# Performance work log

Hardware: AMD Instinct MI355X
Metric: run time of the kernel (lower is better)

Reference implementation:

```python
import jax, jax.numpy as jnp
import numpy as np

NQ = 4  # n_qubits_per_head


def _apply_ry(state, theta, q):
    # state: (N, 2,2,2,2) real amplitudes; theta: (N,) per-element angle; wire q
    st = jnp.moveaxis(state, 1 + q, -1)
    c = jnp.cos(0.5 * theta).reshape(-1, 1, 1, 1)
    s = jnp.sin(0.5 * theta).reshape(-1, 1, 1, 1)
    a0, a1 = st[..., 0], st[..., 1]
    st = jnp.stack([c * a0 - s * a1, s * a0 + c * a1], axis=-1)
    return jnp.moveaxis(st, -1, 1 + q)


def _apply_cnot(state, ctrl, tgt):
    st = jnp.moveaxis(state, (1 + ctrl, 1 + tgt), (-2, -1))
    st = jnp.stack([st[..., 0, :], st[..., 1, ::-1]], axis=-2)
    return jnp.moveaxis(st, (-2, -1), (1 + ctrl, 1 + tgt))


def _quantum_circuit(x_in, par):
    # x_in: (N, NQ) data angles; par: (N, L, NQ) variational angles (per head, tiled)
    N = x_in.shape[0]
    L = par.shape[1]
    state = jnp.zeros((N, 2, 2, 2, 2), x_in.dtype).at[:, 0, 0, 0, 0].set(1.0)
    for l in range(L):
        for q in range(NQ):
            state = _apply_ry(state, par[:, l, q], q)
        for q in range(NQ - 1):
            state = _apply_cnot(state, q, q + 1)
        state = _apply_cnot(state, NQ - 1, 0)
    for q in range(NQ):
        state = _apply_ry(state, x_in[:, q], q)
    p = state * state  # probabilities (real amplitudes: only RY/CNOT gates)
    zs = []
    for q in range(NQ):
        st = jnp.moveaxis(p, 1 + q, -1)
        zs.append(jnp.sum(st[..., 0], axis=(1, 2, 3)) - jnp.sum(st[..., 1], axis=(1, 2, 3)))
    return jnp.stack(zs, axis=-1)  # (N, NQ)


def setup_inputs() -> dict:
    key = jax.random.key(0)
    ks = jax.random.split(key, 6)
    B, T, E, H, L = 4, 2048, 1024, 16, 2
    scale = 1.0 / np.sqrt(E)
    x = jax.random.normal(ks[0], (B, T, E), dtype=jnp.float32)
    Wq = jax.random.normal(ks[1], (E, E), dtype=jnp.float32) * scale
    Wk = jax.random.normal(ks[2], (E, E), dtype=jnp.float32) * scale
    Wv = jax.random.normal(ks[3], (E, E), dtype=jnp.float32) * scale
    Wo = jax.random.normal(ks[4], (E, E), dtype=jnp.float32) * scale
    qparams = jax.random.normal(ks[5], (H, L, NQ), dtype=jnp.float32)
    return {"x": x, "Wq": Wq, "Wk": Wk, "Wv": Wv, "Wo": Wo, "qparams": qparams}


def reference(x, Wq, Wk, Wv, Wo, qparams):
    B, T, E = x.shape
    H, L, _ = qparams.shape
    hd = E // H
    q = x @ Wq.T
    k = x @ Wk.T
    v = x @ Wv.T
    # NOTE: original scales by sqrt(embed_dim), not sqrt(head_dim)
    scores = jnp.einsum('bte,bse->bts', q, k) / jnp.sqrt(jnp.asarray(E, x.dtype))
    w = jax.nn.softmax(scores, axis=-1)
    out = jnp.einsum('bts,bse->bte', w, v)
    oh = out.reshape(B, T, H, hd)
    N = B * T * H
    xin = oh[..., :NQ].reshape(N, NQ)
    par = jnp.broadcast_to(qparams[None, None], (B, T, H, L, NQ)).reshape(N, L, NQ)
    z = _quantum_circuit(xin, par)  # (N, NQ)
    zfull = jnp.concatenate([z, jnp.zeros((N, hd - NQ), x.dtype)], axis=-1)
    return zfull.reshape(B, T, E) @ Wo.T
```

## Files before the change

kernel.cpp:

```cpp
#include <hip/hip_runtime.h>
#include <hip/hip_fp16.h>

typedef _Float16 half_t;
typedef __attribute__((ext_vector_type(4))) _Float16 half4;
typedef __attribute__((ext_vector_type(8))) _Float16 half8;
typedef __attribute__((ext_vector_type(4))) float floatx4;

__device__ __forceinline__ void async_copy16(const void* src, void* dst_lds) {
  __builtin_amdgcn_global_load_lds(
      (__attribute__((address_space(1))) void*)src,
      (__attribute__((address_space(3))) void*)dst_lds, 16, 0, 0);
}

__global__ __launch_bounds__(512, 2) void gemm_nt_256(
    const half_t* __restrict__ A, const half_t* __restrict__ B,
    half_t* __restrict__ C,
    int lda, int ldb, int ldc, int kIters,
    long sAz2, long sBz2, long sCz2, float scale)
{
  __shared__ __align__(16) half_t sm[2][2][256 * 64];

  const int tid  = threadIdx.x;
  const int wave = tid >> 6, lane = tid & 63;
  const int wm = wave >> 2, wn = wave & 3;
  const int er = lane >> 4, ec = lane & 15;
  const int sw = ec & 7;

  const long z = blockIdx.z;
  const half_t* Ab = A + (long)blockIdx.x * 256 * lda + z * sAz2;
  const half_t* Bb = B + (long)blockIdx.y * 256 * ldb + z * sBz2;

  const int srow = tid >> 3;
  const int skq  = (tid & 7) ^ (srow & 7);

  floatx4 acc[2][2][4][2];
  #pragma unroll
  for (int a = 0; a < 2; a++)
    #pragma unroll
    for (int b = 0; b < 2; b++)
      #pragma unroll
      for (int i = 0; i < 4; i++)
        #pragma unroll
        for (int j = 0; j < 2; j++)
          acc[a][b][i][j] = (floatx4){0.f, 0.f, 0.f, 0.f};

#define STAGE_A(bb, hf, kt) do {                                              \
    const half_t* Ak_ = Ab + (long)(kt) * 64;                                 \
    _Pragma("unroll")                                                         \
    for (int r_ = 0; r_ < 2; r_++) {                                          \
      int lrow_ = r_ * 64 + srow;                                             \
      async_copy16(Ak_ + (long)((hf) * 128 + lrow_) * lda + skq * 8,          \
                   &sm[(bb)][0][(hf) * 8192 + (r_ * 512 + wave * 64) * 8]);   \
    } } while (0)

#define STAGE_B(bb, hf, kt) do {                                              \
    const half_t* Bk_ = Bb + (long)(kt) * 64;                                 \
    _Pragma("unroll")                                                         \
    for (int r_ = 0; r_ < 2; r_++) {                                          \
      int lrow_ = r_ * 64 + srow;                                             \
      async_copy16(Bk_ + (long)((hf) * 128 + lrow_) * ldb + skq * 8,          \
                   &sm[(bb)][1][(hf) * 8192 + (r_ * 512 + wave * 64) * 8]);   \
    } } while (0)

#define DS_A(DST, BB, MH, KS) do {                                            \
    _Pragma("unroll")                                                         \
    for (int ii = 0; ii < 4; ii++) {                                          \
      int row_ = (MH) * 128 + wm * 64 + ii * 16 + ec;                         \
      DST[ii] = *(const half8*)                                               \
          &sm[BB][0][row_ * 64 + ((((KS) * 4 + er) ^ sw) * 8)];               \
    } } while (0)

#define DS_B(DST, BB, KS) do {                                                \
    _Pragma("unroll")                                                         \
    for (int nj = 0; nj < 4; nj++) {                                          \
      int row_ = (nj >> 1) * 128 + wn * 32 + (nj & 1) * 16 + ec;              \
      DST[nj] = *(const half8*)                                               \
          &sm[BB][1][row_ * 64 + ((((KS) * 4 + er) ^ sw) * 8)];               \
    } } while (0)

#define MFMA16(AF, BF, MH) do {                                               \
    __builtin_amdgcn_s_setprio(1);                                            \
    _Pragma("unroll")                                                         \
    for (int ii = 0; ii < 4; ii++)                                            \
      _Pragma("unroll")                                                       \
      for (int nj = 0; nj < 4; nj++)                                          \
        acc[MH][nj >> 1][ii][nj & 1] =                                        \
            __builtin_amdgcn_mfma_f32_16x16x32_f16(                           \
                AF[ii], BF[nj], acc[MH][nj >> 1][ii][nj & 1], 0, 0, 0);       \
    __builtin_amdgcn_s_setprio(0);                                            \
  } while (0)

#define BAR() __builtin_amdgcn_s_barrier()
#define VMW(N) asm volatile("s_waitcnt vmcnt(" #N ")" ::: "memory")

  half8 afA[4], afB[4], bfA[4], bfB[4];
  int cur = 0;
  const int nt = kIters;

  STAGE_B(0, 0, 0); STAGE_B(0, 1, 0); STAGE_A(0, 0, 0); STAGE_A(0, 1, 0);
  VMW(2);
  BAR();
  DS_A(afA, 0, 0, 0);
  DS_B(bfA, 0, 0);

  for (int n = 0; n < nt; ++n) {
    const int hasNext = (n + 1 < nt);
    DS_A(afB, cur, 0, 1);
    DS_B(bfB, cur, 1);
    if (hasNext) { STAGE_B(cur ^ 1, 0, n + 1); STAGE_B(cur ^ 1, 1, n + 1); }
    MFMA16(afA, bfA, 0);
    if (hasNext) { VMW(4); } else { VMW(0); }
    BAR();
    DS_A(afA, cur, 1, 0);
    if (hasNext) STAGE_A(cur ^ 1, 0, n + 1);
    MFMA16(afB, bfB, 0);
    BAR();
    DS_A(afB, cur, 1, 1);
    if (hasNext) STAGE_A(cur ^ 1, 1, n + 1);
    MFMA16(afA, bfA, 1);
    if (hasNext) VMW(2);
    BAR();
    if (hasNext) {
      DS_A(afA, cur ^ 1, 0, 0);
      DS_B(bfA, cur ^ 1, 0);
    }
    MFMA16(afB, bfB, 1);
    BAR();
    cur ^= 1;
  }

#undef STAGE_A
#undef STAGE_B
#undef DS_A
#undef DS_B
#undef MFMA16
#undef BAR
#undef VMW

  const long rowBase = (long)blockIdx.x * 256;
  const long colBase = (long)blockIdx.y * 256;
  half_t* Cz = C + z * sCz2;
  #pragma unroll
  for (int mh = 0; mh < 2; mh++)
    #pragma unroll
    for (int nh = 0; nh < 2; nh++)
      #pragma unroll
      for (int ii = 0; ii < 4; ii++)
        #pragma unroll
        for (int jj = 0; jj < 2; jj++)
          #pragma unroll
          for (int r = 0; r < 4; r++) {
            long row = rowBase + mh * 128 + wm * 64 + ii * 16 + er * 4 + r;
            long col = colBase + nh * 128 + wn * 32 + jj * 16 + ec;
            Cz[row * (long)ldc + col] =
                (_Float16)(acc[mh][nh][ii][jj][r] * scale);
          }
}

template<int BN, int EPI>
__global__ __launch_bounds__(256) void gemm_nt(
    const half_t* __restrict__ A, const half_t* __restrict__ B,
    void* __restrict__ Cout,
    int lda, int ldb, int ldc, int kIters, int zShift,
    long sAz1, long sBz1, long sCz1,
    long sAz2, long sBz2, long sCz2, float scale,
    const float* __restrict__ qab)
{
  constexpr int BM = 128;
  constexpr int WN = BN / 2;
  constexpr int AN = WN / 16;
  constexpr int RA = BM * 8 / 256;
  constexpr int RB = BN * 8 / 256;
  __shared__ __align__(16) half_t lA[BM * 64];
  __shared__ __align__(16) half_t lB[BN * 64];

  const int tid  = threadIdx.x;
  const int wave = tid >> 6, lane = tid & 63;
  const int wm = wave >> 1, wn = wave & 1;
  const int er = lane >> 4, ec = lane & 15;
  const int sw = ec & 7;

  const long z = blockIdx.z;
  const long z2 = z >> zShift;
  const long z1 = z - (z2 << zShift);
  const half_t* Ab = A + (long)blockIdx.x * BM * lda + z1 * sAz1 + z2 * sAz2;
  const half_t* Bb = B + (long)blockIdx.y * BN * ldb + z1 * sBz1 + z2 * sBz2;
  const long cz = z1 * sCz1 + z2 * sCz2;

  floatx4 acc[4][AN];
  #pragma unroll
  for (int i = 0; i < 4; i++)
    #pragma unroll
    for (int j = 0; j < AN; j++)
      acc[i][j] = (floatx4){0.f, 0.f, 0.f, 0.f};

  for (int ks = 0; ks < kIters; ++ks) {
    const half_t* Ak = Ab + ks * 64;
    const half_t* Bk = Bb + ks * 64;
    #pragma unroll
    for (int r = 0; r < RA; r++) {
      int s = r * 256 + tid;
      int row = s >> 3;
      int kq = (s & 7) ^ (row & 7);
      async_copy16(Ak + (long)row * lda + kq * 8,
                   &lA[(r * 256 + wave * 64) * 8]);
    }
    #pragma unroll
    for (int r = 0; r < RB; r++) {
      int s = r * 256 + tid;
      int row = s >> 3;
      int kq = (s & 7) ^ (row & 7);
      async_copy16(Bk + (long)row * ldb + kq * 8,
                   &lB[(r * 256 + wave * 64) * 8]);
    }
    __syncthreads();

    #pragma unroll
    for (int h = 0; h < 2; h++) {
      half8 af[4], bfv[AN];
      #pragma unroll
      for (int i = 0; i < 4; i++) {
        int row = wm * 64 + i * 16 + ec;
        af[i] = *(const half8*)&lA[row * 64 + (((h * 4 + er) ^ sw) * 8)];
      }
      #pragma unroll
      for (int j = 0; j < AN; j++) {
        int row = wn * WN + j * 16 + ec;
        bfv[j] = *(const half8*)&lB[row * 64 + (((h * 4 + er) ^ sw) * 8)];
      }
      #pragma unroll
      for (int i = 0; i < 4; i++)
        #pragma unroll
        for (int j = 0; j < AN; j++)
          acc[i][j] = __builtin_amdgcn_mfma_f32_16x16x32_f16(
              af[i], bfv[j], acc[i][j], 0, 0, 0);
    }
    __syncthreads();
  }

  const long rowBase = (long)blockIdx.x * BM + wm * 64;
  const long colBase = (long)blockIdx.y * BN + wn * WN;
  #pragma unroll
  for (int i = 0; i < 4; i++)
    #pragma unroll
    for (int j = 0; j < AN; j++)
      #pragma unroll
      for (int r = 0; r < 4; r++) {
        long row = rowBase + i * 16 + er * 4 + r;
        long col = colBase + j * 16 + ec;
        float v = acc[i][j][r];
        if constexpr (EPI == 0) {
          ((half_t*)Cout)[cz + row * (long)ldc + col] = (_Float16)(v * scale);
        } else if constexpr (EPI == 1) {
          ((half_t*)Cout)[cz + col * (long)ldc + row] = (_Float16)v;
        } else if constexpr (EPI == 2) {
          ((float*)Cout)[cz + row * (long)ldc + col] = v * scale;
        } else if constexpr (EPI == 4) {
          ((float*)Cout)[cz + col * (long)ldc + row] = v;
        } else {
          float za = qab[2 * (int)col], zb = qab[2 * (int)col + 1];
          float zv = za * cosf(v) + zb * sinf(v);
          ((half_t*)Cout)[cz + row * (long)ldc + col] = (_Float16)zv;
        }
      }
}

__global__ __launch_bounds__(256) void pv_softmax(
    const half_t* __restrict__ S, const half_t* __restrict__ V,
    float* __restrict__ Op, float* __restrict__ Lp, int kIters)
{
  __shared__ __align__(16) half_t lA[128 * 64];
  __shared__ __align__(16) half_t lB[64 * 64];

  const int tid  = threadIdx.x;
  const int wave = tid >> 6, lane = tid & 63;
  const int wm = wave >> 1, wn = wave & 1;
  const int er = lane >> 4, ec = lane & 15;
  const int sw = ec & 7;

  const long z = blockIdx.z;
  const long z2 = z >> 2;
  const long z1 = z & 3;
  const half_t* Ab = S + (long)blockIdx.x * 128 * 2048
                       + z1 * ((long)2048 * 2048) + z2 * 512;
  const half_t* Bb = V + z1 * 2048 + z2 * 512;

  floatx4 acc[4][2];
  #pragma unroll
  for (int i = 0; i < 4; i++)
    #pragma unroll
    for (int j = 0; j < 2; j++)
      acc[i][j] = (floatx4){0.f, 0.f, 0.f, 0.f};
  float lsum[4] = {0.f, 0.f, 0.f, 0.f};

  for (int ks = 0; ks < kIters; ++ks) {
    const half_t* Ak = Ab + ks * 64;
    const half_t* Bk = Bb + ks * 64;
    #pragma unroll
    for (int r = 0; r < 4; r++) {
      int s = r * 256 + tid;
      int row = s >> 3;
      int kq = (s & 7) ^ (row & 7);
      async_copy16(Ak + (long)row * 2048 + kq * 8,
                   &lA[(r * 256 + wave * 64) * 8]);
    }
    #pragma unroll
    for (int r = 0; r < 2; r++) {
      int s = r * 256 + tid;
      int row = s >> 3;
      int kq = (s & 7) ^ (row & 7);
      async_copy16(Bk + (long)row * 8192 + kq * 8,
                   &lB[(r * 256 + wave * 64) * 8]);
    }
    __syncthreads();

    #pragma unroll
    for (int h = 0; h < 2; h++) {
      half8 af[4], bfv[2];
      #pragma unroll
      for (int i = 0; i < 4; i++) {
        int row = wm * 64 + i * 16 + ec;
        half8 a = *(const half8*)&lA[row * 64 + (((h * 4 + er) ^ sw) * 8)];
        #pragma unroll
        for (int k = 0; k < 8; k++) {
          float e = __expf((float)a[k]);
          _Float16 ph = (_Float16)e;
          a[k] = ph;
          lsum[i] += (float)ph;
        }
        af[i] = a;
      }
      #pragma unroll
      for (int j = 0; j < 2; j++) {
        int row = wn * 32 + j * 16 + ec;
        bfv[j] = *(const half8*)&lB[row * 64 + (((h * 4 + er) ^ sw) * 8)];
      }
      #pragma unroll
      for (int i = 0; i < 4; i++)
        #pragma unroll
        for (int j = 0; j < 2; j++)
          acc[i][j] = __builtin_amdgcn_mfma_f32_16x16x32_f16(
              af[i], bfv[j], acc[i][j], 0, 0, 0);
    }
    __syncthreads();
  }

  const long zo = z2 * ((long)8192 * 64) + z1 * ((long)2048 * 64);
  const long rowBase = (long)blockIdx.x * 128 + wm * 64;
  #pragma unroll
  for (int i = 0; i < 4; i++)
    #pragma unroll
    for (int j = 0; j < 2; j++)
      #pragma unroll
      for (int r = 0; r < 4; r++) {
        long row = rowBase + i * 16 + er * 4 + r;
        long col = wn * 32 + j * 16 + ec;
        Op[zo + row * 64 + col] = acc[i][j][r];
      }

  const long lb = z2 * 8192 + z1 * 2048 + (long)blockIdx.x * 128 + wm * 64;
  #pragma unroll
  for (int i = 0; i < 4; i++) {
    float v = lsum[i];
    v += __shfl_xor(v, 16);
    v += __shfl_xor(v, 32);
    if (wn == 0 && er == 0) Lp[lb + i * 16 + ec] = v;
  }
}

__global__ __launch_bounds__(256) void v4_reduce(const float* __restrict__ P,
                                                 half_t* __restrict__ O)
{
  const long CH = (long)64 * 8192;
  long i = ((long)blockIdx.x * 256 + threadIdx.x) * 4;
  float4 a = *(const float4*)(P + i);
  float4 b = *(const float4*)(P + i + CH);
  float4 c = *(const float4*)(P + i + 2 * CH);
  float4 d = *(const float4*)(P + i + 3 * CH);
  half4 o;
  o[0] = (_Float16)(a.x + b.x + c.x + d.x);
  o[1] = (_Float16)(a.y + b.y + c.y + d.y);
  o[2] = (_Float16)(a.z + b.z + c.z + d.z);
  o[3] = (_Float16)(a.w + b.w + c.w + d.w);
  *(half4*)(O + i) = o;
}

__global__ __launch_bounds__(256) void z_reduce_quantum(
    const float* __restrict__ P, const float* __restrict__ Lp,
    const float* __restrict__ qab, half_t* __restrict__ O)
{
  const long CH = (long)8192 * 64;
  long i = ((long)blockIdx.x * 256 + threadIdx.x) * 4;
  long t = i >> 6;
  float4 a = *(const float4*)(P + i);
  float4 b = *(const float4*)(P + i + CH);
  float4 c = *(const float4*)(P + i + 2 * CH);
  float4 d = *(const float4*)(P + i + 3 * CH);
  float l = Lp[t] + Lp[8192 + t] + Lp[2 * 8192 + t] + Lp[3 * 8192 + t];
  float inv = 1.f / l;
  float s[4] = {(a.x + b.x + c.x + d.x) * inv, (a.y + b.y + c.y + d.y) * inv,
                (a.z + b.z + c.z + d.z) * inv, (a.w + b.w + c.w + d.w) * inv};
  int c0 = (int)(i & 63);
  half4 o;
  #pragma unroll
  for (int j = 0; j < 4; j++) {
    float za = qab[2 * (c0 + j)], zb = qab[2 * (c0 + j) + 1];
    o[j] = (_Float16)(za * cosf(s[j]) + zb * sinf(s[j]));
  }
  *(half4*)(O + i) = o;
}

__global__ __launch_bounds__(256) void softmax_rows(half_t* __restrict__ S,
                                                    int ld)
{
  const long row = blockIdx.x;
  half8* sp = (half8*)(S + row * (long)ld);
  const int t = threadIdx.x;
  const int wave = t >> 6, lane = t & 63;
  half8 hv = sp[t];
  float e[8];
  #pragma unroll
  for (int k = 0; k < 8; k++) e[k] = (float)hv[k];
  float m = e[0];
  #pragma unroll
  for (int k = 1; k < 8; k++) m = fmaxf(m, e[k]);
  #pragma unroll
  for (int o = 32; o > 0; o >>= 1) m = fmaxf(m, __shfl_xor(m, o));
  __shared__ float rmax[4], rsum[4];
  if (lane == 0) rmax[wave] = m;
  __syncthreads();
  m = fmaxf(fmaxf(rmax[0], rmax[1]), fmaxf(rmax[2], rmax[3]));
  float s = 0.f;
  #pragma unroll
  for (int k = 0; k < 8; k++) { e[k] = expf(e[k] - m); s += e[k]; }
  #pragma unroll
  for (int o = 32; o > 0; o >>= 1) s += __shfl_xor(s, o);
  if (lane == 0) rsum[wave] = s;
  __syncthreads();
  float inv = 1.f / (rsum[0] + rsum[1] + rsum[2] + rsum[3]);
  half8 o8;
  #pragma unroll
  for (int k = 0; k < 8; k++) o8[k] = (_Float16)(e[k] * inv);
  sp[t] = o8;
}

__global__ __launch_bounds__(256) void prep_all(
    const float* __restrict__ x,  const float* __restrict__ Wq,
    const float* __restrict__ Wk, const float* __restrict__ Wv,
    const float* __restrict__ Wo, const float* __restrict__ qp, int L,
    half_t* __restrict__ xh, half_t* __restrict__ Wqk,
    half_t* __restrict__ Wv4, half_t* __restrict__ Wos,
    float* __restrict__ qab)
{
  const int bid = blockIdx.x;
  if (bid < 4096) {
    long i = ((long)bid * 256 + threadIdx.x) * 8;
    float4 a = *(const float4*)(x + i);
    float4 b = *(const float4*)(x + i + 4);
    half8 h = {(_Float16)a.x, (_Float16)a.y, (_Float16)a.z, (_Float16)a.w,
               (_Float16)b.x, (_Float16)b.y, (_Float16)b.z, (_Float16)b.w};
    *(half8*)(xh + i) = h;
  } else if (bid < 5120) {
    long i = ((long)(bid - 4096) * 256 + threadIdx.x) * 8;
    int r = (int)(i >> 10);
    int e = (int)(i & 1023);
    const float* src = (r < 1024 ? Wq + (long)r * 1024
                                 : Wk + (long)(r - 1024) * 1024) + e;
    float4 a = *(const float4*)src;
    float4 b = *(const float4*)(src + 4);
    half8 h = {(_Float16)a.x, (_Float16)a.y, (_Float16)a.z, (_Float16)a.w,
               (_Float16)b.x, (_Float16)b.y, (_Float16)b.z, (_Float16)b.w};
    *(half8*)(Wqk + i) = h;
  } else if (bid < 5152) {
    long i = ((long)(bid - 5120) * 256 + threadIdx.x) * 8;
    int c = (int)(i >> 10);
    int e = (int)(i & 1023);
    const float* src = Wv + (long)(((c >> 2) << 6) | (c & 3)) * 1024 + e;
    float4 a = *(const float4*)src;
    float4 b = *(const float4*)(src + 4);
    half8 h = {(_Float16)a.x, (_Float16)a.y, (_Float16)a.z, (_Float16)a.w,
               (_Float16)b.x, (_Float16)b.y, (_Float16)b.z, (_Float16)b.w};
    *(half8*)(Wv4 + i) = h;
  } else if (bid < 5408) {
    int idx = (bid - 5152) * 256 + threadIdx.x;
    int e = idx >> 6, c = idx & 63;
    Wos[idx] = (_Float16)Wo[(long)e * 1024 + (((c >> 2) << 6) | (c & 3))];
  } else {
    int h = threadIdx.x;
    if (h >= 16) return;
    float st[16];
    #pragma unroll
    for (int i = 0; i < 16; i++) st[i] = 0.f;
    st[0] = 1.f;
    for (int l = 0; l < L; l++) {
      #pragma unroll
      for (int q = 0; q < 4; q++) {
        float th = qp[(h * L + l) * 4 + q];
        float c = cosf(0.5f * th), s = sinf(0.5f * th);
        int mq = 8 >> q;
        #pragma unroll
        for (int i = 0; i < 16; i++) {
          if ((i & mq) == 0) {
            float a0 = st[i], a1 = st[i | mq];
            st[i]      = c * a0 - s * a1;
            st[i | mq] = s * a0 + c * a1;
          }
        }
      }
      const int cm[4] = {8, 4, 2, 1};
      const int tm[4] = {4, 2, 1, 8};
      #pragma unroll
      for (int p = 0; p < 4; p++) {
        int mc = cm[p], mt = tm[p];
        #pragma unroll
        for (int i = 0; i < 16; i++) {
          if ((i & mc) != 0 && (i & mt) == 0) {
            float tv = st[i]; st[i] = st[i | mt]; st[i | mt] = tv;
          }
        }
      }
    }
    #pragma unroll
    for (int q = 0; q < 4; q++) {
      int mq = 8 >> q;
      float zc = 0.f, xc = 0.f;
      #pragma unroll
      for (int i = 0; i < 16; i++) {
        float p2 = st[i] * st[i];
        zc += ((i & mq) == 0) ? p2 : -p2;
        if ((i & mq) == 0) xc += st[i] * st[i | mq];
      }
      qab[(h * 4 + q) * 2 + 0] = zc;
      qab[(h * 4 + q) * 2 + 1] = -2.f * xc;
    }
  }
}

extern "C" void kernel_launch(void* const* d_in, const int* in_sizes, int n_in,
                              void* d_out, int out_size, void* d_ws, size_t ws_size,
                              hipStream_t stream)
{
  const float* x  = (const float*)d_in[0];
  const float* Wq = (const float*)d_in[1];
  const float* Wk = (const float*)d_in[2];
  const float* Wv = (const float*)d_in[3];
  const float* Wo = (const float*)d_in[4];
  const float* qp = (const float*)d_in[5];
  const int L = in_sizes[5] / 64;
  float* out = (float*)d_out;

  char* w = (char*)d_ws;
  size_t off = 0;
  auto alloc = [&](size_t bytes) -> void* {
    void* p = w + off;
    off = (off + bytes + 255) & ~(size_t)255;
    return p;
  };
  float*  qab  = (float*)alloc(512);
  half_t* xh   = (half_t*)alloc((size_t)8192 * 1024 * 2);
  half_t* Wqk  = (half_t*)alloc((size_t)2048 * 1024 * 2);
  half_t* Wv4  = (half_t*)alloc((size_t)64 * 1024 * 2);
  half_t* Wos  = (half_t*)alloc((size_t)1024 * 64 * 2);
  half_t* V4th = (half_t*)alloc((size_t)64 * 8192 * 2);
  half_t* Z4   = (half_t*)alloc((size_t)8192 * 64 * 2);
  float*  Lp   = (float*)alloc((size_t)4 * 8192 * 4);

  half_t* QKb = (half_t*)d_out;

  int tier = (ws_size >= off + (size_t)8192 * 2048 * 2 + 256) ? 0 : 1;
  const size_t Sn = (tier == 0) ? (size_t)8192 * 2048 : (size_t)2048 * 2048;
  half_t* S = (half_t*)alloc(Sn * 2);

  prep_all<<<dim3(5409), dim3(256), 0, stream>>>(
      x, Wq, Wk, Wv, Wo, qp, L, xh, Wqk, Wv4, Wos, qab);

  gemm_nt_256<<<dim3(32, 8, 1), 512, 0, stream>>>(
      xh, Wqk, QKb, 1024, 1024, 2048, 16, 0, 0, 0, 1.f);

  if (tier == 0) {
    float* V4p = (float*)S;
    gemm_nt<64, 4><<<dim3(64, 1, 4), 256, 0, stream>>>(
        xh, Wv4, V4p, 1024, 1024, 8192, 4, 0,
        0, 0, 0, 256, 256, (long)64 * 8192, 1.f, nullptr);
    v4_reduce<<<dim3(512), dim3(256), 0, stream>>>(V4p, V4th);

    gemm_nt_256<<<dim3(8, 8, 4), 512, 0, stream>>>(
        QKb, QKb + 1024, S, 2048, 2048, 2048, 16,
        (long)2048 * 2048, (long)2048 * 2048, (long)2048 * 2048, 0.03125f);

    float* Zp = (float*)d_out;
    pv_softmax<<<dim3(16, 1, 16), 256, 0, stream>>>(S, V4th, Zp, Lp, 8);
    z_reduce_quantum<<<dim3(512), dim3(256), 0, stream>>>(Zp, Lp, qab, Z4);
  } else {
    gemm_nt<64, 1><<<dim3(64, 1, 1), 256, 0, stream>>>(
        xh, Wv4, V4th, 1024, 1024, 8192, 16, 0,
        0, 0, 0, 0, 0, 0, 1.f, nullptr);
    for (int b = 0; b < 4; b++) {
      const long q0 = (long)b * 2048;
      gemm_nt<128, 0><<<dim3(16, 16, 1), 256, 0, stream>>>(
          QKb + q0 * 2048, QKb + 1024 + q0 * 2048, S,
          2048, 2048, 2048, 16, 0, 0, 0, 0, 0, 0, 0, 0.03125f, nullptr);
      softmax_rows<<<dim3(2048), dim3(256), 0, stream>>>(S, 2048);
      gemm_nt<64, 5><<<dim3(16, 1, 1), 256, 0, stream>>>(
          S, V4th + q0, Z4 + q0 * 64, 2048, 8192, 64, 32, 0,
          0, 0, 0, 0, 0, 0, 1.f, qab);
    }
  }

  gemm_nt<128, 2><<<dim3(64, 8, 1), 256, 0, stream>>>(
      Z4, Wos, out, 64, 64, 1024, 1, 0,
      0, 0, 0, 0, 0, 0, 1.f, nullptr);
}
```

Measured before the change: 213.4 us.

## Restructure GEMM main loop into quadrant-wise LDS loads with full-K fragments

Reorganizes the 256x256 GEMM inner loop so each phase loads the A or B fragments for both k-substeps of one output quadrant, then issues the MFMAs for that quadrant, reusing the A fragments across two N halves and the B fragments across two M halves. The staging order of the async global-to-LDS copies is re-interleaved to match, and explicit lgkmcnt(0) waits plus extra barriers are added before each MFMA batch. This aims to cut redundant LDS fragment reads and give a more regular load/compute schedule. In exchange it adds barriers and full LDS waits, which may expose LDS latency that the old double-buffered register fragments hid, and it holds more fragment registers.

```diff
diff --git a/kernel.cpp b/kernel.cpp
--- a/kernel.cpp
+++ b/kernel.cpp
@@ -62,69 +62,75 @@
                    &sm[(bb)][1][(hf) * 8192 + (r_ * 512 + wave * 64) * 8]);   \
     } } while (0)
 
-#define DS_A(DST, BB, MH, KS) do {                                            \
+#define DS_A(DST, BB, MH) do {                                                \
     _Pragma("unroll")                                                         \
     for (int ii = 0; ii < 4; ii++) {                                          \
       int row_ = (MH) * 128 + wm * 64 + ii * 16 + ec;                         \
-      DST[ii] = *(const half8*)                                               \
-          &sm[BB][0][row_ * 64 + ((((KS) * 4 + er) ^ sw) * 8)];               \
+      _Pragma("unroll")                                                       \
+      for (int ks = 0; ks < 2; ks++)                                          \
+        DST[ii][ks] = *(const half8*)                                         \
+            &sm[BB][0][row_ * 64 + (((ks * 4 + er) ^ sw) * 8)];               \
     } } while (0)
 
-#define DS_B(DST, BB, KS) do {                                                \
+#define DS_B(DST, BB, NH) do {                                                \
     _Pragma("unroll")                                                         \
-    for (int nj = 0; nj < 4; nj++) {                                          \
-      int row_ = (nj >> 1) * 128 + wn * 32 + (nj & 1) * 16 + ec;              \
-      DST[nj] = *(const half8*)                                               \
-          &sm[BB][1][row_ * 64 + ((((KS) * 4 + er) ^ sw) * 8)];               \
+    for (int jj = 0; jj < 2; jj++) {                                          \
+      int row_ = (NH) * 128 + wn * 32 + jj * 16 + ec;                         \
+      _Pragma("unroll")                                                       \
+      for (int ks = 0; ks < 2; ks++)                                          \
+        DST[jj][ks] = *(const half8*)                                         \
+            &sm[BB][1][row_ * 64 + (((ks * 4 + er) ^ sw) * 8)];               \
     } } while (0)
 
-#define MFMA16(AF, BF, MH) do {                                               \
+#define MFMA_Q(AF, BF, MH, NH) do {                                           \
     __builtin_amdgcn_s_setprio(1);                                            \
     _Pragma("unroll")                                                         \
-    for (int ii = 0; ii < 4; ii++)                                            \
+    for (int ks = 0; ks < 2; ks++)                                            \
       _Pragma("unroll")                                                       \
-      for (int nj = 0; nj < 4; nj++)                                          \
-        acc[MH][nj >> 1][ii][nj & 1] =                                        \
-            __builtin_amdgcn_mfma_f32_16x16x32_f16(                           \
-                AF[ii], BF[nj], acc[MH][nj >> 1][ii][nj & 1], 0, 0, 0);       \
+      for (int ii = 0; ii < 4; ii++)                                          \
+        _Pragma("unroll")                                                     \
+        for (int jj = 0; jj < 2; jj++)                                        \
+          acc[MH][NH][ii][jj] = __builtin_amdgcn_mfma_f32_16x16x32_f16(       \
+              AF[ii][ks], BF[jj][ks], acc[MH][NH][ii][jj], 0, 0, 0);          \
     __builtin_amdgcn_s_setprio(0);                                            \
   } while (0)
 
 #define BAR() __builtin_amdgcn_s_barrier()
+#define LGKM0() do { asm volatile("s_waitcnt lgkmcnt(0)" ::: "memory");       \
+                     __builtin_amdgcn_sched_barrier(0); } while (0)
 #define VMW(N) asm volatile("s_waitcnt vmcnt(" #N ")" ::: "memory")
 
-  half8 afA[4], afB[4], bfA[4], bfB[4];
+  half8 afX[4][2], bfX[2][2], bfY[2][2];
   int cur = 0;
   const int nt = kIters;
 
-  STAGE_B(0, 0, 0); STAGE_B(0, 1, 0); STAGE_A(0, 0, 0); STAGE_A(0, 1, 0);
-  VMW(2);
+  STAGE_A(0, 0, 0); STAGE_B(0, 0, 0); STAGE_B(0, 1, 0); STAGE_A(0, 1, 0);
+  VMW(4);
   BAR();
-  DS_A(afA, 0, 0, 0);
-  DS_B(bfA, 0, 0);
 
   for (int n = 0; n < nt; ++n) {
     const int hasNext = (n + 1 < nt);
-    DS_A(afB, cur, 0, 1);
-    DS_B(bfB, cur, 1);
-    if (hasNext) { STAGE_B(cur ^ 1, 0, n + 1); STAGE_B(cur ^ 1, 1, n + 1); }
-    MFMA16(afA, bfA, 0);
+    DS_A(afX, cur, 0);
+    DS_B(bfX, cur, 0);
+    if (hasNext) STAGE_A(cur ^ 1, 0, n + 1);
+    BAR(); LGKM0();
+    MFMA_Q(afX, bfX, 0, 0);
     if (hasNext) { VMW(4); } else { VMW(0); }
     BAR();
-    DS_A(afA, cur, 1, 0);
-    if (hasNext) STAGE_A(cur ^ 1, 0, n + 1);
-    MFMA16(afB, bfB, 0);
+    DS_B(bfY, cur, 1);
+    if (hasNext) STAGE_B(cur ^ 1, 0, n + 1);
+    BAR(); LGKM0();
+    MFMA_Q(afX, bfY, 0, 1);
+    if (hasNext) VMW(4);
     BAR();
-    DS_A(afB, cur, 1, 1);
+    DS_A(afX, cur, 1);
+    if (hasNext) STAGE_B(cur ^ 1, 1, n + 1);
+    BAR(); LGKM0();
+    MFMA_Q(afX, bfY, 1, 1);
+    BAR();
     if (hasNext) STAGE_A(cur ^ 1, 1, n + 1);
-    MFMA16(afA, bfA, 1);
-    if (hasNext) VMW(2);
-    BAR();
-    if (hasNext) {
-      DS_A(afA, cur ^ 1, 0, 0);
-      DS_B(bfA, cur ^ 1, 0);
-    }
-    MFMA16(afB, bfB, 1);
+    MFMA_Q(afX, bfX, 1, 0);
+    if (hasNext) VMW(4);
     BAR();
     cur ^= 1;
   }
@@ -133,8 +139,9 @@
 #undef STAGE_B
 #undef DS_A
 #undef DS_B
-#undef MFMA16
+#undef MFMA_Q
 #undef BAR
+#undef LGKM0
 #undef VMW
 
   const long rowBase = (long)blockIdx.x * 256;
```

New measurement: 211.8 us. About the same (-0.8%).
